# Kernel tuning notes

Measured on AMD Instinct MI355X. Metric: run time of the kernel, lower is better.

## Reference

```python
import jax, jax.numpy as jnp
import numpy as np

CLS_NUM = 2
SF = 8.0
STRIDE = 5
NO_OBJ_SCALE = 1.0
GAMMA = 1.0
B, C, H, W = 16, 8, 256, 256
NT = 256


def setup_inputs() -> dict:
    key = jax.random.key(0)
    k1, k2, k3, k4, k5, k6, k7 = jax.random.split(key, 7)
    predict = jax.random.normal(k1, (B, C, H, W), dtype=jnp.float32)
    b = jax.random.randint(k2, (NT,), 0, B).astype(jnp.float32)
    c = jax.random.randint(k3, (NT,), 0, CLS_NUM).astype(jnp.float32)
    cx = jax.random.uniform(k4, (NT,)) * (W * SF)   # image-scale coords
    cy = jax.random.uniform(k5, (NT,)) * (H * SF)
    wh = jax.random.uniform(k6, (NT, 2)) * 72.0 + 8.0  # box sizes in [8,80] px
    ang = (jax.random.uniform(k7, (NT,)) - 0.5) * np.pi
    targets = jnp.stack([b, c, cx, cy, wh[:, 0], wh[:, 1], ang], axis=1).astype(jnp.float32)
    return {"predict": predict, "targets": targets}


def _forward_loss(predict, targets):
    nB, nC, nH, nW = predict.shape
    N = targets.shape[0]
    pred = jnp.transpose(predict, (0, 2, 3, 1))  # [B,H,W,C]
    half = (STRIDE - 1) / 2.0
    x = jax.nn.sigmoid(pred[..., 0]) * STRIDE - half
    y = jax.nn.sigmoid(pred[..., 1]) * STRIDE - half
    w_p = pred[..., 2]
    h_p = pred[..., 3]
    p = jax.nn.sigmoid(pred[..., 4]) * 2.0 - 1.0
    q = jax.nn.sigmoid(pred[..., 5]) * 2.0 - 1.0

    # targets are detached in the torch code (numpy) -> no grad path
    tg = jax.lax.stop_gradient(targets)
    b_idx = tg[:, 0].astype(jnp.int32)
    cls_t = tg[:, 1].astype(jnp.int32)
    cx = tg[:, 2] / SF
    cy = tg[:, 3] / SF
    bw = tg[:, 4] / SF
    bh = tg[:, 5] / SF
    ang = tg[:, 6]
    ca, sa = jnp.cos(ang), jnp.sin(ang)

    # --- rotated-box rasterization for all boxes at once: [N,H,W] ---
    gx = jnp.arange(nW, dtype=jnp.float32) + 0.5
    gy = jnp.arange(nH, dtype=jnp.float32) + 0.5
    vx = gx[None, None, :] * ca[:, None, None] + gy[None, :, None] * sa[:, None, None]
    vy = -gx[None, None, :] * sa[:, None, None] + gy[None, :, None] * ca[:, None, None]
    bx = cx * ca + cy * sa
    by = -cx * sa + cy * ca
    x3 = (bx - bh / 2)[:, None, None]
    x4 = (bx + bh / 2)[:, None, None]
    y3 = (by - bw / 2)[:, None, None]
    y4 = (by + bw / 2)[:, None, None]
    inbox = (vx >= x3) & (vx <= x4) & (vy >= y3) & (vy <= y4)
    inexp = (vx >= x3 - 0.5) & (vx <= x4 + 0.5) & (vy >= y3 - 0.5) & (vy <= y4 + 0.5)

    # --- candidate grid cells around each box center (stride+1 window) ---
    lower = 0.5 - STRIDE / 2.0  # -2.0
    upper = 0.5 + STRIDE / 2.0  # 3.0
    K = STRIDE + 1
    i0 = jnp.floor(cx + lower).astype(jnp.int32)
    j0 = jnp.floor(cy + lower).astype(jnp.int32)
    I = jnp.broadcast_to((i0[:, None] + jnp.arange(K))[:, None, :], (N, K, K))
    J = jnp.broadcast_to((j0[:, None] + jnp.arange(K))[:, :, None], (N, K, K))
    ox = cx[:, None, None] - I.astype(jnp.float32)
    oy = cy[:, None, None] - J.astype(jnp.float32)
    inb = (I >= 0) & (I < nW) & (J >= 0) & (J < nH)
    off = (ox >= lower) & (ox <= upper) & (oy >= lower) & (oy <= upper)
    Ic = jnp.clip(I, 0, nW - 1)
    Jc = jnp.clip(J, 0, nH - 1)
    lin = ((b_idx[:, None, None] * nH + Jc) * nW + Ic).reshape(-1)
    SIZE = nB * nH * nW
    oxf = ox.reshape(-1)
    oyf = oy.reshape(-1)
    logw_f = jnp.broadcast_to(jnp.log(bw)[:, None, None], (N, K, K)).reshape(-1)
    logh_f = jnp.broadcast_to(jnp.log(bh)[:, None, None], (N, K, K)).reshape(-1)
    ang_f = jnp.broadcast_to(ang[:, None, None], (N, K, K)).reshape(-1)
    vflat = jnp.minimum(jnp.abs(oxf - 0.5), jnp.abs(oyf - 0.5))  # assignment priority

    total = jnp.float32(0.0)
    for c_id in range(CLS_NUM):
        cm = cls_t == c_id
        heat = jax.ops.segment_sum((inbox & cm[:, None, None]).astype(jnp.float32), b_idx, num_segments=nB) > 0
        cold = jax.ops.segment_sum((inexp & cm[:, None, None]).astype(jnp.float32), b_idx, num_segments=nB) == 0
        validf = (inb & off & cm[:, None, None]).reshape(-1)
        heat_at = heat.reshape(-1)[lin]
        cold_at = cold.reshape(-1)[lin]
        # noobj cleared at window cells overlapping the expanded rotated boxes
        clear_idx = jnp.where(validf & ~cold_at, lin, SIZE)
        noobj = jnp.ones(SIZE + 1, jnp.float32).at[clear_idx].set(0.0)[:SIZE]
        # per-cell min-priority box assignment (scatter-min + winner gather)
        elig = validf & heat_at
        vbig = jnp.where(elig, vflat, jnp.inf)
        minv = jnp.full(SIZE, jnp.inf, jnp.float32).at[lin].min(vbig)
        win = elig & (vbig <= minv[lin])
        widx = jnp.where(win, lin, SIZE)

        def scat(vals):
            return jnp.zeros(SIZE + 1, jnp.float32).at[widx].set(vals)[:SIZE]

        obj = jnp.zeros(SIZE + 1, jnp.float32).at[widx].set(1.0)[:SIZE]
        tx = scat(oxf).reshape(nB, nH, nW)
        ty = scat(oyf).reshape(nB, nH, nW)
        tw = scat(logw_f).reshape(nB, nH, nW)
        th = scat(logh_f).reshape(nB, nH, nW)
        ta = scat(ang_f).reshape(nB, nH, nW)
        obj = obj.reshape(nB, nH, nW)
        noobj = (noobj.reshape(nB, nH, nW)) * (1.0 - obj)

        n_obj = jnp.sum(obj)
        dn = jnp.maximum(n_obj, 1.0)
        n_no = jnp.sum(noobj)
        dno = jnp.maximum(n_no, 1.0)
        z = pred[..., 6 + c_id]  # conf logit; BCE(sigmoid(z), t) == softplus(+/-z)
        loss_conf_obj = jnp.sum(obj * jax.nn.softplus(-z)) / dn
        loss_conf_noobj = jnp.sum(noobj * jax.nn.softplus(z)) / dno

        def om(t):
            return jnp.sum(obj * t) / dn

        loss_x = om((x - tx) ** 2)
        loss_y = om((y - ty) ** 2)
        loss_w = om((w_p - tw) ** 2)
        loss_h = om((h_p - th) ** 2)
        wt = th - tw  # log(h)-log(w) at obj cells
        awt = jnp.abs(wt) ** GAMMA
        loss_angle = om(awt * (jnp.abs(p - jnp.cos(2.0 * ta)) + jnp.abs(q - jnp.sin(2.0 * ta))))
        loss_ring = om(jnp.abs(wt) * jnp.abs(p * p + q * q - 1.0))
        cls_loss = (loss_conf_obj + NO_OBJ_SCALE * loss_conf_noobj
                    + loss_x + loss_y + loss_w + loss_h + loss_angle + loss_ring)
        total = total + jnp.where(n_obj > 0, cls_loss, 0.0)
    return total


def reference(predict, targets):
    return _forward_loss(predict, targets)
```

## Files before the change

### kernel.cpp

```cpp
#include <hip/hip_runtime.h>
#include <math.h>

#define NTGT 256
#define NB 16
#define NH 256
#define NW 256
#define GSIZE (NB * NH * NW)

#define NCONFBLK 256
#define NENTBLK 36
#define NBLK (NCONFBLK + NENTBLK)
#define MAGIC 0x5EC0FFEEu

typedef unsigned long long u64;

#define PART64 0
#define ENT64  256

__device__ __forceinline__ float softplusf(float z) {
    return fmaxf(z, 0.0f) + log1pf(expf(-fabsf(z)));
}
__device__ __forceinline__ float sigmoidf(float t) {
    return 1.0f / (1.0f + expf(-t));
}
__device__ __forceinline__ void pub(u64* p, float v) {
    const u64 w = ((u64)MAGIC << 32) | (u64)__float_as_uint(v);
    __hip_atomic_store(p, w, __ATOMIC_RELAXED, __HIP_MEMORY_SCOPE_AGENT);
}
__device__ __forceinline__ float poll(const u64* p) {
    u64 x = __hip_atomic_load(p, __ATOMIC_RELAXED, __HIP_MEMORY_SCOPE_AGENT);
    while ((unsigned)(x >> 32) != MAGIC) {
        __builtin_amdgcn_s_sleep(1);
        x = __hip_atomic_load(p, __ATOMIC_RELAXED, __HIP_MEMORY_SCOPE_AGENT);
    }
    return __uint_as_float((unsigned)x);
}

__global__ __launch_bounds__(256) void fused_all(const float* __restrict__ predict,
                                                 const float* __restrict__ targets,
                                                 u64* __restrict__ ws,
                                                 float* __restrict__ out) {
#pragma clang fp contract(off)
    __shared__ float s_raw[NTGT * 7];
    __shared__ float s_cx[NTGT], s_cy[NTGT], s_ca[NTGT], s_sa[NTGT];
    __shared__ float s_x3[NTGT], s_x4[NTGT], s_y3[NTGT], s_y4[NTGT];
    __shared__ int   s_i0[NTGT], s_j0[NTGT], s_g[NTGT], s_gl[NTGT];
    __shared__ int   s_gs[33];
    __shared__ int   cntg[32];
    __shared__ float blksum[16];
    __shared__ unsigned blkcnt[4];

    const int t = threadIdx.x;
    const int bid = blockIdx.x;

    if (bid < NCONFBLK) {
        const int cb = bid;
        const int j = cb * 256 + t;
        const int ch  = 6 + ((j >> 14) & 1);
        const int pos = j & 16383;
        const int bhi = j >> 15;
        float s = 0.0f;
        for (int it = 0; it < 8; ++it) {
            const int b = it * 2 + bhi;
            const float4 v = *reinterpret_cast<const float4*>(
                predict + (size_t)(b * 8 + ch) * 65536 + (size_t)pos * 4);
            s += softplusf(v.x) + softplusf(v.y) + softplusf(v.z) + softplusf(v.w);
        }
        for (int o = 32; o > 0; o >>= 1) s += __shfl_down(s, o, 64);
        if ((t & 63) == 0) blksum[t >> 6] = s;
        __syncthreads();
        if (t == 0)
            pub(&ws[PART64 + cb], blksum[0] + blksum[1] + blksum[2] + blksum[3]);
        return;
    }

    const int eb = bid - NCONFBLK;
    for (int i = t; i < NTGT * 7; i += 256) s_raw[i] = targets[i];
    if (t < 32) cntg[t] = 0;
    if (t < 16) blksum[t] = 0.0f;
    if (t >= 16 && t < 20) blkcnt[t - 16] = 0u;
    __syncthreads();

    {
        const float* T = &s_raw[t * 7];
        const int b   = (int)T[0];
        const int cls = (int)T[1];
        const float cx = T[2] * 0.125f, cy = T[3] * 0.125f;
        const float bw = T[4] * 0.125f, bh = T[5] * 0.125f;
        float sa, ca;
        sincosf(T[6], &sa, &ca);
        const float bx =  cx * ca + cy * sa;
        const float by = -cx * sa + cy * ca;
        const int g = b * 2 + cls;
        s_cx[t] = cx;  s_cy[t] = cy;
        s_ca[t] = ca;  s_sa[t] = sa;
        s_x3[t] = bx - bh * 0.5f;  s_x4[t] = bx + bh * 0.5f;
        s_y3[t] = by - bw * 0.5f;  s_y4[t] = by + bw * 0.5f;
        s_i0[t] = (int)floorf(cx - 2.0f);
        s_j0[t] = (int)floorf(cy - 2.0f);
        s_g[t]  = g;
        const int pos = atomicAdd(&cntg[g], 1);
        __syncthreads();
        if (t < 32) {
            int sc = cntg[t];
            for (int o = 1; o < 32; o <<= 1) {
                const int u = __shfl_up(sc, o, 64);
                if (t >= o) sc += u;
            }
            s_gs[t + 1] = sc;
            if (t == 0) s_gs[0] = 0;
        }
        __syncthreads();
        s_gl[s_gs[g] + pos] = t;
    }
    __syncthreads();

    const int e = eb * 256 + t;
    const int n = e / 36;
    const int sub = e - n * 36;
    const int kj = sub / 6;
    const int ki = sub - kj * 6;

    const int g = s_g[n];
    const int cls = g & 1;
    const int b = g >> 1;
    const int I = s_i0[n] + ki, J = s_j0[n] + kj;
    const float cx = s_cx[n], cy = s_cy[n];
    const float ox = cx - (float)I;
    const float oy = cy - (float)J;

    const bool validf = (I >= 0 && I < NW && J >= 0 && J < NH) &&
                        (ox >= -2.0f && ox <= 3.0f && oy >= -2.0f && oy <= 3.0f);

    bool isOwner = false, isWinC = false;
    const int gs = s_gs[g], ge = s_gs[g + 1];
    if (validf) {
        const float vfl = fminf(fabsf(ox - 0.5f), fabsf(oy - 0.5f));
        const unsigned long long mypack =
            ((unsigned long long)__float_as_uint(vfl) << 32) | (unsigned)e;
        unsigned long long best = mypack;
        int ownmin = e;
        for (int p = gs; p < ge; ++p) {
            const int m = s_gl[p];
            if (m == n) continue;
            const int kip = I - s_i0[m];
            if (kip < 0 || kip > 5) continue;
            const int kjp = J - s_j0[m];
            if (kjp < 0 || kjp > 5) continue;
            const float oxp = s_cx[m] - (float)I;
            const float oyp = s_cy[m] - (float)J;
            if (!(oxp >= -2.0f && oxp <= 3.0f && oyp >= -2.0f && oyp <= 3.0f)) continue;
            const int ep = (m * 6 + kjp) * 6 + kip;
            ownmin = min(ownmin, ep);
            const float vflp = fminf(fabsf(oxp - 0.5f), fabsf(oyp - 0.5f));
            const unsigned long long pk =
                ((unsigned long long)__float_as_uint(vflp) << 32) | (unsigned)ep;
            if (pk < best) best = pk;
        }
        isOwner = (ownmin == e);
        isWinC  = (best == mypack);
    }

    bool heat = false, anyexp = false;
    if (isOwner || isWinC) {
        const float gx = (float)I + 0.5f;
        const float gy = (float)J + 0.5f;
        for (int p = gs; p < ge; ++p) {
            const int m = s_gl[p];
            const float ca = s_ca[m], sa = s_sa[m];
            const float vx =  gx * ca + gy * sa;
            const float vy = -gx * sa + gy * ca;
            const float x3 = s_x3[m], x4 = s_x4[m];
            const float y3 = s_y3[m], y4 = s_y4[m];
            heat   |= (vx >= x3 && vx <= x4 && vy >= y3 && vy <= y4);
            anyexp |= (vx >= x3 - 0.5f && vx <= x4 + 0.5f &&
                       vy >= y3 - 0.5f && vy <= y4 + 0.5f);
        }
    }

    const size_t base = (size_t)b * 8 * 65536 + (size_t)J * 256 + (size_t)I;
    const bool doClear = isOwner && anyexp;
    const bool doWin   = isWinC && heat;

    float spz = 0.0f;
    if (doClear) spz = softplusf(predict[base + (size_t)(6 + cls) * 65536]);
    float v0 = (doClear && cls == 0) ? spz : 0.0f;
    float v1 = (doClear && cls == 1) ? spz : 0.0f;
    for (int o = 32; o > 0; o >>= 1) {
        v0 += __shfl_down(v0, o, 64);
        v1 += __shfl_down(v1, o, 64);
    }
    const unsigned long long m0 = __ballot(doClear && cls == 0);
    const unsigned long long m1 = __ballot(doClear && cls == 1);
    if ((t & 63) == 0) {
        if (v0 != 0.0f) atomicAdd(&blksum[14], v0);
        if (v1 != 0.0f) atomicAdd(&blksum[15], v1);
        if (m0) atomicAdd(&blkcnt[2], (unsigned)__popcll(m0));
        if (m1) atomicAdd(&blkcnt[3], (unsigned)__popcll(m1));
    }

    if (doWin) {
        const float p0 = predict[base];
        const float p1 = predict[base + 65536];
        const float p2 = predict[base + 2 * 65536];
        const float p3 = predict[base + 3 * 65536];
        const float p4 = predict[base + 4 * 65536];
        const float p5 = predict[base + 5 * 65536];
        const float z  = predict[base + (size_t)(6 + cls) * 65536];
        const float bw = s_raw[n * 7 + 4] * 0.125f;
        const float bh = s_raw[n * 7 + 5] * 0.125f;
        const float ang = s_raw[n * 7 + 6];
        const float xs = sigmoidf(p0) * 5.0f - 2.0f;
        const float ys = sigmoidf(p1) * 5.0f - 2.0f;
        const float pp = sigmoidf(p4) * 2.0f - 1.0f;
        const float qq = sigmoidf(p5) * 2.0f - 1.0f;
        const float tw = logf(bw), th = logf(bh);
        const float wt = th - tw, awt = fabsf(wt);
        float s2a, c2a;
        sincosf(2.0f * ang, &s2a, &c2a);
        atomicAdd(&blksum[0 + cls],  softplusf(-z));
        atomicAdd(&blksum[2 + cls],  (xs - ox) * (xs - ox));
        atomicAdd(&blksum[4 + cls],  (ys - oy) * (ys - oy));
        atomicAdd(&blksum[6 + cls],  (p2 - tw) * (p2 - tw));
        atomicAdd(&blksum[8 + cls],  (p3 - th) * (p3 - th));
        atomicAdd(&blksum[10 + cls], awt * (fabsf(pp - c2a) + fabsf(qq - s2a)));
        atomicAdd(&blksum[12 + cls], awt * fabsf(pp * pp + qq * qq - 1.0f));
        atomicAdd(&blkcnt[cls], 1u);
    }

    __syncthreads();
    if (t < 16) {
        pub(&ws[ENT64 + eb * 20 + t], blksum[t]);
    } else if (t < 20) {
        pub(&ws[ENT64 + eb * 20 + t], (float)blkcnt[t - 16]);
    }

    if (bid != NBLK - 1) return;

    if (t < 20) s_sa[t] = 0.0f;
    const float v = poll(&ws[PART64 + t]);
    const int c = (t >> 6) & 1;
    s_cx[t] = c ? 0.0f : v;
    s_cy[t] = c ? v : 0.0f;
    __syncthreads();
    for (int idx = t; idx < NENTBLK * 20; idx += 256) {
        atomicAdd(&s_sa[idx % 20], poll(&ws[ENT64 + idx]));
    }
    for (int o = 128; o > 0; o >>= 1) {
        __syncthreads();
        if (t < o) { s_cx[t] += s_cx[t + o]; s_cy[t] += s_cy[t + o]; }
    }
    __syncthreads();
    if (t == 0) {
        const float sAll[2] = { s_cx[0], s_cy[0] };
        float total = 0.0f;
        for (int c2 = 0; c2 < 2; ++c2) {
            const float nobj = s_sa[16 + c2];
            if (nobj > 0.0f) {
                const float dn  = nobj;
                const float dno = fmaxf((float)GSIZE - s_sa[18 + c2], 1.0f);
                total += s_sa[0 + c2] / dn
                       + (sAll[c2] - s_sa[14 + c2]) / dno
                       + (s_sa[2 + c2] + s_sa[4 + c2] + s_sa[6 + c2]
                          + s_sa[8 + c2] + s_sa[10 + c2] + s_sa[12 + c2]) / dn;
            }
        }
        out[0] = total;
    }
}

extern "C" void kernel_launch(void* const* d_in, const int* in_sizes, int n_in,
                              void* d_out, int out_size, void* d_ws, size_t ws_size,
                              hipStream_t stream) {
    const float* predict = (const float*)d_in[0];
    const float* targets = (const float*)d_in[1];
    float* out = (float*)d_out;
    u64* ws = (u64*)d_ws;

    fused_all<<<NBLK, 256, 0, stream>>>(predict, targets, ws, out);
}
```

Measured before the change: 19.27 us.

## Merge conf and entry work into one block set; batch final polling

```diff
diff --git a/kernel.cpp b/kernel.cpp
--- a/kernel.cpp
+++ b/kernel.cpp
@@ -7,15 +7,17 @@
 #define NW 256
 #define GSIZE (NB * NH * NW)
 
-#define NCONFBLK 256
-#define NENTBLK 36
-#define NBLK (NCONFBLK + NENTBLK)
+#define NBLK 256
+#define NENTBLK 72
+#define ENTPB 128
 #define MAGIC 0x5EC0FFEEu
 
 typedef unsigned long long u64;
 
 #define PART64 0
 #define ENT64  256
+#define NWORDS (256 + NENTBLK * 20)
+#define POLLK  7
 
 __device__ __forceinline__ float softplusf(float z) {
     return fmaxf(z, 0.0f) + log1pf(expf(-fabsf(z)));
@@ -27,13 +29,8 @@
     const u64 w = ((u64)MAGIC << 32) | (u64)__float_as_uint(v);
     __hip_atomic_store(p, w, __ATOMIC_RELAXED, __HIP_MEMORY_SCOPE_AGENT);
 }
-__device__ __forceinline__ float poll(const u64* p) {
-    u64 x = __hip_atomic_load(p, __ATOMIC_RELAXED, __HIP_MEMORY_SCOPE_AGENT);
-    while ((unsigned)(x >> 32) != MAGIC) {
-        __builtin_amdgcn_s_sleep(1);
-        x = __hip_atomic_load(p, __ATOMIC_RELAXED, __HIP_MEMORY_SCOPE_AGENT);
-    }
-    return __uint_as_float((unsigned)x);
+__device__ __forceinline__ u64 rd64(const u64* p) {
+    return __hip_atomic_load(p, __ATOMIC_RELAXED, __HIP_MEMORY_SCOPE_AGENT);
 }
 
 __global__ __launch_bounds__(256) void fused_all(const float* __restrict__ predict,
@@ -47,15 +44,16 @@
     __shared__ int   s_i0[NTGT], s_j0[NTGT], s_g[NTGT], s_gl[NTGT];
     __shared__ int   s_gs[33];
     __shared__ int   cntg[32];
+    __shared__ float red4[4];
     __shared__ float blksum[16];
     __shared__ unsigned blkcnt[4];
+    __shared__ float fsum[22];
 
     const int t = threadIdx.x;
     const int bid = blockIdx.x;
 
-    if (bid < NCONFBLK) {
-        const int cb = bid;
-        const int j = cb * 256 + t;
+    {
+        const int j = bid * 256 + t;
         const int ch  = 6 + ((j >> 14) & 1);
         const int pos = j & 16383;
         const int bhi = j >> 15;
@@ -67,14 +65,14 @@
             s += softplusf(v.x) + softplusf(v.y) + softplusf(v.z) + softplusf(v.w);
         }
         for (int o = 32; o > 0; o >>= 1) s += __shfl_down(s, o, 64);
-        if ((t & 63) == 0) blksum[t >> 6] = s;
+        if ((t & 63) == 0) red4[t >> 6] = s;
         __syncthreads();
         if (t == 0)
-            pub(&ws[PART64 + cb], blksum[0] + blksum[1] + blksum[2] + blksum[3]);
-        return;
-    }
-
-    const int eb = bid - NCONFBLK;
+            pub(&ws[PART64 + bid], red4[0] + red4[1] + red4[2] + red4[3]);
+    }
+
+    if (bid >= NENTBLK) return;
+
     for (int i = t; i < NTGT * 7; i += 256) s_raw[i] = targets[i];
     if (t < 32) cntg[t] = 0;
     if (t < 16) blksum[t] = 0.0f;
@@ -115,154 +113,180 @@
     }
     __syncthreads();
 
-    const int e = eb * 256 + t;
-    const int n = e / 36;
-    const int sub = e - n * 36;
-    const int kj = sub / 6;
-    const int ki = sub - kj * 6;
-
-    const int g = s_g[n];
-    const int cls = g & 1;
-    const int b = g >> 1;
-    const int I = s_i0[n] + ki, J = s_j0[n] + kj;
-    const float cx = s_cx[n], cy = s_cy[n];
-    const float ox = cx - (float)I;
-    const float oy = cy - (float)J;
-
-    const bool validf = (I >= 0 && I < NW && J >= 0 && J < NH) &&
-                        (ox >= -2.0f && ox <= 3.0f && oy >= -2.0f && oy <= 3.0f);
-
-    bool isOwner = false, isWinC = false;
-    const int gs = s_gs[g], ge = s_gs[g + 1];
-    if (validf) {
-        const float vfl = fminf(fabsf(ox - 0.5f), fabsf(oy - 0.5f));
-        const unsigned long long mypack =
-            ((unsigned long long)__float_as_uint(vfl) << 32) | (unsigned)e;
-        unsigned long long best = mypack;
-        int ownmin = e;
-        for (int p = gs; p < ge; ++p) {
-            const int m = s_gl[p];
-            if (m == n) continue;
-            const int kip = I - s_i0[m];
-            if (kip < 0 || kip > 5) continue;
-            const int kjp = J - s_j0[m];
-            if (kjp < 0 || kjp > 5) continue;
-            const float oxp = s_cx[m] - (float)I;
-            const float oyp = s_cy[m] - (float)J;
-            if (!(oxp >= -2.0f && oxp <= 3.0f && oyp >= -2.0f && oyp <= 3.0f)) continue;
-            const int ep = (m * 6 + kjp) * 6 + kip;
-            ownmin = min(ownmin, ep);
-            const float vflp = fminf(fabsf(oxp - 0.5f), fabsf(oyp - 0.5f));
-            const unsigned long long pk =
-                ((unsigned long long)__float_as_uint(vflp) << 32) | (unsigned)ep;
-            if (pk < best) best = pk;
-        }
-        isOwner = (ownmin == e);
-        isWinC  = (best == mypack);
-    }
-
-    bool heat = false, anyexp = false;
-    if (isOwner || isWinC) {
-        const float gx = (float)I + 0.5f;
-        const float gy = (float)J + 0.5f;
-        for (int p = gs; p < ge; ++p) {
-            const int m = s_gl[p];
-            const float ca = s_ca[m], sa = s_sa[m];
-            const float vx =  gx * ca + gy * sa;
-            const float vy = -gx * sa + gy * ca;
-            const float x3 = s_x3[m], x4 = s_x4[m];
-            const float y3 = s_y3[m], y4 = s_y4[m];
-            heat   |= (vx >= x3 && vx <= x4 && vy >= y3 && vy <= y4);
-            anyexp |= (vx >= x3 - 0.5f && vx <= x4 + 0.5f &&
-                       vy >= y3 - 0.5f && vy <= y4 + 0.5f);
-        }
-    }
-
-    const size_t base = (size_t)b * 8 * 65536 + (size_t)J * 256 + (size_t)I;
-    const bool doClear = isOwner && anyexp;
-    const bool doWin   = isWinC && heat;
-
-    float spz = 0.0f;
-    if (doClear) spz = softplusf(predict[base + (size_t)(6 + cls) * 65536]);
-    float v0 = (doClear && cls == 0) ? spz : 0.0f;
-    float v1 = (doClear && cls == 1) ? spz : 0.0f;
-    for (int o = 32; o > 0; o >>= 1) {
-        v0 += __shfl_down(v0, o, 64);
-        v1 += __shfl_down(v1, o, 64);
-    }
-    const unsigned long long m0 = __ballot(doClear && cls == 0);
-    const unsigned long long m1 = __ballot(doClear && cls == 1);
-    if ((t & 63) == 0) {
-        if (v0 != 0.0f) atomicAdd(&blksum[14], v0);
-        if (v1 != 0.0f) atomicAdd(&blksum[15], v1);
-        if (m0) atomicAdd(&blkcnt[2], (unsigned)__popcll(m0));
-        if (m1) atomicAdd(&blkcnt[3], (unsigned)__popcll(m1));
-    }
-
-    if (doWin) {
-        const float p0 = predict[base];
-        const float p1 = predict[base + 65536];
-        const float p2 = predict[base + 2 * 65536];
-        const float p3 = predict[base + 3 * 65536];
-        const float p4 = predict[base + 4 * 65536];
-        const float p5 = predict[base + 5 * 65536];
-        const float z  = predict[base + (size_t)(6 + cls) * 65536];
-        const float bw = s_raw[n * 7 + 4] * 0.125f;
-        const float bh = s_raw[n * 7 + 5] * 0.125f;
-        const float ang = s_raw[n * 7 + 6];
-        const float xs = sigmoidf(p0) * 5.0f - 2.0f;
-        const float ys = sigmoidf(p1) * 5.0f - 2.0f;
-        const float pp = sigmoidf(p4) * 2.0f - 1.0f;
-        const float qq = sigmoidf(p5) * 2.0f - 1.0f;
-        const float tw = logf(bw), th = logf(bh);
-        const float wt = th - tw, awt = fabsf(wt);
-        float s2a, c2a;
-        sincosf(2.0f * ang, &s2a, &c2a);
-        atomicAdd(&blksum[0 + cls],  softplusf(-z));
-        atomicAdd(&blksum[2 + cls],  (xs - ox) * (xs - ox));
-        atomicAdd(&blksum[4 + cls],  (ys - oy) * (ys - oy));
-        atomicAdd(&blksum[6 + cls],  (p2 - tw) * (p2 - tw));
-        atomicAdd(&blksum[8 + cls],  (p3 - th) * (p3 - th));
-        atomicAdd(&blksum[10 + cls], awt * (fabsf(pp - c2a) + fabsf(qq - s2a)));
-        atomicAdd(&blksum[12 + cls], awt * fabsf(pp * pp + qq * qq - 1.0f));
-        atomicAdd(&blkcnt[cls], 1u);
+    if (t < ENTPB) {
+        const int e = bid * ENTPB + t;
+        const int n = e / 36;
+        const int sub = e - n * 36;
+        const int kj = sub / 6;
+        const int ki = sub - kj * 6;
+
+        const int g = s_g[n];
+        const int cls = g & 1;
+        const int b = g >> 1;
+        const int I = s_i0[n] + ki, J = s_j0[n] + kj;
+        const float cx = s_cx[n], cy = s_cy[n];
+        const float ox = cx - (float)I;
+        const float oy = cy - (float)J;
+
+        const bool validf = (I >= 0 && I < NW && J >= 0 && J < NH) &&
+                            (ox >= -2.0f && ox <= 3.0f && oy >= -2.0f && oy <= 3.0f);
+
+        bool isOwner = false, isWinC = false;
+        const int gs = s_gs[g], ge = s_gs[g + 1];
+        if (validf) {
+            const float vfl = fminf(fabsf(ox - 0.5f), fabsf(oy - 0.5f));
+            const u64 mypack = ((u64)__float_as_uint(vfl) << 32) | (unsigned)e;
+            u64 best = mypack;
+            int ownmin = e;
+            for (int p = gs; p < ge; ++p) {
+                const int m = s_gl[p];
+                if (m == n) continue;
+                const int kip = I - s_i0[m];
+                if (kip < 0 || kip > 5) continue;
+                const int kjp = J - s_j0[m];
+                if (kjp < 0 || kjp > 5) continue;
+                const float oxp = s_cx[m] - (float)I;
+                const float oyp = s_cy[m] - (float)J;
+                if (!(oxp >= -2.0f && oxp <= 3.0f && oyp >= -2.0f && oyp <= 3.0f)) continue;
+                const int ep = (m * 6 + kjp) * 6 + kip;
+                ownmin = min(ownmin, ep);
+                const float vflp = fminf(fabsf(oxp - 0.5f), fabsf(oyp - 0.5f));
+                const u64 pk = ((u64)__float_as_uint(vflp) << 32) | (unsigned)ep;
+                if (pk < best) best = pk;
+            }
+            isOwner = (ownmin == e);
+            isWinC  = (best == mypack);
+        }
+
+        bool heat = false, anyexp = false;
+        if (isOwner || isWinC) {
+            const float gx = (float)I + 0.5f;
+            const float gy = (float)J + 0.5f;
+            for (int p = gs; p < ge; ++p) {
+                const int m = s_gl[p];
+                const float ca = s_ca[m], sa = s_sa[m];
+                const float vx =  gx * ca + gy * sa;
+                const float vy = -gx * sa + gy * ca;
+                const float x3 = s_x3[m], x4 = s_x4[m];
+                const float y3 = s_y3[m], y4 = s_y4[m];
+                heat   |= (vx >= x3 && vx <= x4 && vy >= y3 && vy <= y4);
+                anyexp |= (vx >= x3 - 0.5f && vx <= x4 + 0.5f &&
+                           vy >= y3 - 0.5f && vy <= y4 + 0.5f);
+            }
+        }
+
+        const size_t base = (size_t)b * 8 * 65536 + (size_t)J * 256 + (size_t)I;
+        const bool doClear = isOwner && anyexp;
+        const bool doWin   = isWinC && heat;
+
+        float spz = 0.0f;
+        if (doClear) spz = softplusf(predict[base + (size_t)(6 + cls) * 65536]);
+        float v0 = (doClear && cls == 0) ? spz : 0.0f;
+        float v1 = (doClear && cls == 1) ? spz : 0.0f;
+        for (int o = 32; o > 0; o >>= 1) {
+            v0 += __shfl_down(v0, o, 64);
+            v1 += __shfl_down(v1, o, 64);
+        }
+        const u64 m0 = __ballot(doClear && cls == 0);
+        const u64 m1 = __ballot(doClear && cls == 1);
+        if ((t & 63) == 0) {
+            if (v0 != 0.0f) atomicAdd(&blksum[14], v0);
+            if (v1 != 0.0f) atomicAdd(&blksum[15], v1);
+            if (m0) atomicAdd(&blkcnt[2], (unsigned)__popcll(m0));
+            if (m1) atomicAdd(&blkcnt[3], (unsigned)__popcll(m1));
+        }
+
+        if (doWin) {
+            const float p0 = predict[base];
+            const float p1 = predict[base + 65536];
+            const float p2 = predict[base + 2 * 65536];
+            const float p3 = predict[base + 3 * 65536];
+            const float p4 = predict[base + 4 * 65536];
+            const float p5 = predict[base + 5 * 65536];
+            const float z  = predict[base + (size_t)(6 + cls) * 65536];
+            const float bw = s_raw[n * 7 + 4] * 0.125f;
+            const float bh = s_raw[n * 7 + 5] * 0.125f;
+            const float ang = s_raw[n * 7 + 6];
+            const float xs = sigmoidf(p0) * 5.0f - 2.0f;
+            const float ys = sigmoidf(p1) * 5.0f - 2.0f;
+            const float pp = sigmoidf(p4) * 2.0f - 1.0f;
+            const float qq = sigmoidf(p5) * 2.0f - 1.0f;
+            const float tw = logf(bw), th = logf(bh);
+            const float wt = th - tw, awt = fabsf(wt);
+            float s2a, c2a;
+            sincosf(2.0f * ang, &s2a, &c2a);
+            atomicAdd(&blksum[0 + cls],  softplusf(-z));
+            atomicAdd(&blksum[2 + cls],  (xs - ox) * (xs - ox));
+            atomicAdd(&blksum[4 + cls],  (ys - oy) * (ys - oy));
+            atomicAdd(&blksum[6 + cls],  (p2 - tw) * (p2 - tw));
+            atomicAdd(&blksum[8 + cls],  (p3 - th) * (p3 - th));
+            atomicAdd(&blksum[10 + cls], awt * (fabsf(pp - c2a) + fabsf(qq - s2a)));
+            atomicAdd(&blksum[12 + cls], awt * fabsf(pp * pp + qq * qq - 1.0f));
+            atomicAdd(&blkcnt[cls], 1u);
+        }
     }
 
     __syncthreads();
     if (t < 16) {
-        pub(&ws[ENT64 + eb * 20 + t], blksum[t]);
+        pub(&ws[ENT64 + bid * 20 + t], blksum[t]);
     } else if (t < 20) {
-        pub(&ws[ENT64 + eb * 20 + t], (float)blkcnt[t - 16]);
-    }
-
-    if (bid != NBLK - 1) return;
-
-    if (t < 20) s_sa[t] = 0.0f;
-    const float v = poll(&ws[PART64 + t]);
-    const int c = (t >> 6) & 1;
-    s_cx[t] = c ? 0.0f : v;
-    s_cy[t] = c ? v : 0.0f;
-    __syncthreads();
-    for (int idx = t; idx < NENTBLK * 20; idx += 256) {
-        atomicAdd(&s_sa[idx % 20], poll(&ws[ENT64 + idx]));
-    }
-    for (int o = 128; o > 0; o >>= 1) {
-        __syncthreads();
-        if (t < o) { s_cx[t] += s_cx[t + o]; s_cy[t] += s_cy[t + o]; }
-    }
-    __syncthreads();
+        pub(&ws[ENT64 + bid * 20 + t], (float)blkcnt[t - 16]);
+    }
+
+    if (bid != 0) return;
+
+    if (t < 22) fsum[t] = 0.0f;
+    __syncthreads();
+
+    u64 val[POLLK];
+    bool rdy[POLLK];
+#pragma unroll
+    for (int k = 0; k < POLLK; ++k) {
+        const int w = t + k * 256;
+        if (w < NWORDS) {
+            val[k] = rd64(&ws[w]);
+            rdy[k] = ((unsigned)(val[k] >> 32) == MAGIC);
+        } else {
+            rdy[k] = true;
+        }
+    }
+    for (;;) {
+        bool all = true;
+#pragma unroll
+        for (int k = 0; k < POLLK; ++k) all &= rdy[k];
+        if (all) break;
+        __builtin_amdgcn_s_sleep(1);
+#pragma unroll
+        for (int k = 0; k < POLLK; ++k) {
+            const int w = t + k * 256;
+            if (!rdy[k]) {
+                val[k] = rd64(&ws[w]);
+                rdy[k] = ((unsigned)(val[k] >> 32) == MAGIC);
+            }
+        }
+    }
+#pragma unroll
+    for (int k = 0; k < POLLK; ++k) {
+        const int w = t + k * 256;
+        if (w < NWORDS) {
+            const float v = __uint_as_float((unsigned)val[k]);
+            const int slot = (w < 256) ? ((w >> 6) & 1) : (2 + (w - 256) % 20);
+            atomicAdd(&fsum[slot], v);
+        }
+    }
+    __syncthreads();
+
     if (t == 0) {
-        const float sAll[2] = { s_cx[0], s_cy[0] };
         float total = 0.0f;
-        for (int c2 = 0; c2 < 2; ++c2) {
-            const float nobj = s_sa[16 + c2];
+        for (int c = 0; c < 2; ++c) {
+            const float nobj = fsum[2 + 16 + c];
             if (nobj > 0.0f) {
                 const float dn  = nobj;
-                const float dno = fmaxf((float)GSIZE - s_sa[18 + c2], 1.0f);
-                total += s_sa[0 + c2] / dn
-                       + (sAll[c2] - s_sa[14 + c2]) / dno
-                       + (s_sa[2 + c2] + s_sa[4 + c2] + s_sa[6 + c2]
-                          + s_sa[8 + c2] + s_sa[10 + c2] + s_sa[12 + c2]) / dn;
+                const float dno = fmaxf((float)GSIZE - fsum[2 + 18 + c], 1.0f);
+                total += fsum[2 + 0 + c] / dn
+                       + (fsum[c] - fsum[2 + 14 + c]) / dno
+                       + (fsum[2 + 2 + c] + fsum[2 + 4 + c] + fsum[2 + 6 + c]
+                          + fsum[2 + 8 + c] + fsum[2 + 10 + c] + fsum[2 + 12 + c]) / dn;
             }
         }
         out[0] = total;
```

New measurement: 26.16 us. +35.8%, slower.
